# Performance work log

Hardware: AMD Instinct MI355X
Metric: run time of the kernel (lower is better)

The kernel has to match this reference:

```python
import jax, jax.numpy as jnp
import numpy as np

B = 16384
DENSE_IN = 512
N_SPARSE = 26
EMB = 128
OUT_DIM = 512
NI = N_SPARSE + 1  # 27 rows in interaction matrix
DOT_OUT = NI * (NI + 1) // 2 + DENSE_IN  # 378 + 512 = 890


def setup_inputs() -> dict:
    key = jax.random.key(0)
    ks = jax.random.split(key, 6)
    dense_tensor = jax.random.normal(ks[0], (B, DENSE_IN), dtype=jnp.float32)
    sparse_tensor = jax.random.normal(ks[1], (B, N_SPARSE, EMB), dtype=jnp.float32)
    # nn.Linear(DENSE_IN, EMB): weight [EMB, DENSE_IN], bias [EMB]
    Wp = jax.random.normal(ks[2], (EMB, DENSE_IN), dtype=jnp.float32) * (1.0 / np.sqrt(DENSE_IN))
    bp = jax.random.normal(ks[3], (EMB,), dtype=jnp.float32) * 0.01
    # nn.Linear(DOT_OUT, OUT_DIM): weight [OUT_DIM, DOT_OUT], bias [OUT_DIM]
    Wo = jax.random.normal(ks[4], (OUT_DIM, DOT_OUT), dtype=jnp.float32) * (1.0 / np.sqrt(DOT_OUT))
    bo = jax.random.normal(ks[5], (OUT_DIM,), dtype=jnp.float32) * 0.01
    return {"dense_tensor": dense_tensor, "sparse_tensor": sparse_tensor,
            "Wp": Wp, "bp": bp, "Wo": Wo, "bo": bo}


def reference(dense_tensor, sparse_tensor, Wp, bp, Wo, bo):
    # Project dense feature into embedding space (dims differ in this config)
    dense_proj = dense_tensor @ Wp.T + bp                      # [B, EMB]
    T = jnp.concatenate([dense_proj[:, None, :], sparse_tensor], axis=1)  # [B, NI, EMB]
    Z = jnp.einsum('bie,bje->bij', T, T)                       # [B, NI, NI]
    li, lj = jnp.tril_indices(NI)                              # include diagonal (offset=0)
    Zflat = Z[:, li, lj]                                       # [B, NI*(NI+1)/2]
    Zflat = jnp.concatenate([dense_tensor, Zflat], axis=-1)    # [B, DOT_OUT]
    out = Zflat @ Wo.T + bo                                    # [B, OUT_DIM]
    return out
```

## Files before the change

kernel.cpp:

```cpp
#include <hip/hip_runtime.h>

#define NB    16384
#define DIN   512
#define NSP   26
#define EMBD  128
#define NOUT  512
#define NI_   27
#define NTRI  378
#define DOTK  890
#define KPAD  896

typedef __attribute__((ext_vector_type(8)))  short bf16x8;
typedef __attribute__((ext_vector_type(4)))  float f32x4;

__device__ __forceinline__ short f2bf(float f) {
    unsigned u = __builtin_bit_cast(unsigned, f);
    unsigned r = (u + 0x7FFFu + ((u >> 16) & 1u)) >> 16;
    return (short)r;
}

__device__ __forceinline__ bf16x8 cvt8(float4 a, float4 b) {
    bf16x8 r;
    r[0] = f2bf(a.x); r[1] = f2bf(a.y); r[2] = f2bf(a.z); r[3] = f2bf(a.w);
    r[4] = f2bf(b.x); r[5] = f2bf(b.y); r[6] = f2bf(b.z); r[7] = f2bf(b.w);
    return r;
}

__device__ __forceinline__ void gld_lds16(const void* g, void* l) {
    __builtin_amdgcn_global_load_lds((const __attribute__((address_space(1))) void*)g,
                                     (__attribute__((address_space(3))) void*)l,
                                     16, 0, 0);
}

#define CONV_N2  (NB * 64)
#define WOP_N2   (NOUT * (KPAD / 8))
#define WPB_N2   (EMBD * DIN / 8)
__global__ __launch_bounds__(256) void prep_all_k(const float* __restrict__ dense,
                                                  const float* __restrict__ Wo,
                                                  const float* __restrict__ Wp,
                                                  short* __restrict__ zfb,
                                                  short* __restrict__ wop,
                                                  short* __restrict__ wpb) {
    int idx = blockIdx.x * 256 + threadIdx.x;
    if (idx < CONV_N2) {
        int b = idx >> 6, c = (idx & 63) * 8;
        const float4* p = (const float4*)(dense + (size_t)b * DIN + c);
        *(bf16x8*)(zfb + (size_t)b * KPAD + c) = cvt8(p[0], p[1]);
    } else if (idx < CONV_N2 + WOP_N2) {
        int j = idx - CONV_N2;
        int o = j / (KPAD / 8), rem = j - o * (KPAD / 8);
        int k = rem * 8;
        const float* src = Wo + (size_t)o * DOTK + k;
        bf16x8 r;
#pragma unroll
        for (int t = 0; t < 8; ++t) r[t] = (k + t < DOTK) ? f2bf(src[t]) : (short)0;
        *(bf16x8*)(wop + (size_t)o * KPAD + k) = r;
    } else {
        int j = idx - CONV_N2 - WOP_N2;
        if (j < WPB_N2) {
            const float4* p = (const float4*)(Wp + (size_t)j * 8);
            *(bf16x8*)(wpb + (size_t)j * 8) = cvt8(p[0], p[1]);
        }
    }
}

template <int BM, int BN, bool OUTBF, int GXL2>
__global__ __launch_bounds__(256) void gemm_mfma(const short* __restrict__ A, int lda,
                                                 const short* __restrict__ Bm, int ldb,
                                                 const float* __restrict__ bias,
                                                 void* __restrict__ Cp, int ldc, int K) {
    constexpr int WM = BM / 2, WN = BN / 2;
    constexpr int MT = WM / 16, NT = WN / 16;
    __shared__ short As[BM * 64];
    __shared__ short Bs[BN * 64];

    const int tid = threadIdx.x;
    const int w = tid >> 6, l = tid & 63;
    const int wm = w >> 1, wn = w & 1;
    const int r0 = l & 15, q = l >> 4;

    const int nwg = (int)(gridDim.y << GXL2);
    const int bid = ((int)blockIdx.y << GXL2) | (int)blockIdx.x;
    const int swz = (bid & 7) * (nwg >> 3) + (bid >> 3);
    const int m0 = (swz >> GXL2) * BM;
    const int n0 = (swz & ((1 << GXL2) - 1)) * BN;

    const int lr = l >> 3, pseg = l & 7;

    const f32x4 zero4 = {0.f, 0.f, 0.f, 0.f};
    f32x4 acc[MT][NT];
#pragma unroll
    for (int mi = 0; mi < MT; ++mi)
#pragma unroll
        for (int ni = 0; ni < NT; ++ni) acc[mi][ni] = zero4;

    for (int k0 = 0; k0 < K; k0 += 64) {
#pragma unroll
        for (int i = 0; i < BM / 32; ++i) {
            int r = w * (BM / 4) + i * 8 + lr;
            int ls = pseg ^ (r & 7);
            gld_lds16(A + (size_t)(m0 + r) * lda + k0 + ls * 8,
                      (char*)As + (w * (BM / 4) + i * 8) * 128);
        }
#pragma unroll
        for (int i = 0; i < BN / 32; ++i) {
            int r = w * (BN / 4) + i * 8 + lr;
            int ls = pseg ^ (r & 7);
            gld_lds16(Bm + (size_t)(n0 + r) * ldb + k0 + ls * 8,
                      (char*)Bs + (w * (BN / 4) + i * 8) * 128);
        }
        __syncthreads();

#pragma unroll
        for (int h = 0; h < 2; ++h) {
            bf16x8 af[MT], bfr[NT];
#pragma unroll
            for (int mi = 0; mi < MT; ++mi) {
                int r = wm * WM + mi * 16 + r0;
                af[mi] = *(const bf16x8*)&As[r * 64 + ((h * 4 + q) ^ (r & 7)) * 8];
            }
#pragma unroll
            for (int ni = 0; ni < NT; ++ni) {
                int r = wn * WN + ni * 16 + r0;
                bfr[ni] = *(const bf16x8*)&Bs[r * 64 + ((h * 4 + q) ^ (r & 7)) * 8];
            }
#pragma unroll
            for (int mi = 0; mi < MT; ++mi)
#pragma unroll
                for (int ni = 0; ni < NT; ++ni)
                    acc[mi][ni] = __builtin_amdgcn_mfma_f32_16x16x32_bf16(
                        af[mi], bfr[ni], acc[mi][ni], 0, 0, 0);
        }
        __syncthreads();
    }

#pragma unroll
    for (int mi = 0; mi < MT; ++mi) {
#pragma unroll
        for (int ni = 0; ni < NT; ++ni) {
            int col = n0 + wn * WN + ni * 16 + r0;
            float bb = bias[col];
#pragma unroll
            for (int r = 0; r < 4; ++r) {
                int row = m0 + wm * WM + mi * 16 + q * 4 + r;
                float v = acc[mi][ni][r] + bb;
                if (OUTBF) ((short*)Cp)[(size_t)row * ldc + col] = f2bf(v);
                else       ((float*)Cp)[(size_t)row * ldc + col] = v;
            }
        }
    }
}

__global__ __launch_bounds__(256) void interact_mfma(const float* __restrict__ sparse,
                                                     const short* __restrict__ dprojb,
                                                     short* __restrict__ zfb) {
    __shared__ short zt[4][384];
    const int w = threadIdx.x >> 6, l = threadIdx.x & 63;
    const int b = blockIdx.x * 4 + w;
    const int r0 = l & 15, q = l >> 4;

    const float* srow = sparse + (size_t)b * (NSP * EMBD);
    const short* dp = dprojb + (size_t)b * EMBD;

    const f32x4 zero4 = {0.f, 0.f, 0.f, 0.f};
    f32x4 acc00 = zero4, acc10 = zero4, acc11 = zero4;

#pragma unroll
    for (int kc = 0; kc < 4; ++kc) {
        int k = kc * 32 + q * 8;
        bf16x8 f0, f1;
        if (r0 == 0) {
            f0 = *(const bf16x8*)(dp + k);
        } else {
            const float* p = srow + (size_t)(r0 - 1) * EMBD + k;
            f0 = cvt8(*(const float4*)p, *(const float4*)(p + 4));
        }
        if (r0 <= 10) {
            const float* p = srow + (size_t)(15 + r0) * EMBD + k;
            f1 = cvt8(*(const float4*)p, *(const float4*)(p + 4));
        } else {
            f1 = (bf16x8){0, 0, 0, 0, 0, 0, 0, 0};
        }
        acc00 = __builtin_amdgcn_mfma_f32_16x16x32_bf16(f0, f0, acc00, 0, 0, 0);
        acc10 = __builtin_amdgcn_mfma_f32_16x16x32_bf16(f1, f0, acc10, 0, 0, 0);
        acc11 = __builtin_amdgcn_mfma_f32_16x16x32_bf16(f1, f1, acc11, 0, 0, 0);
    }

#pragma unroll
    for (int r = 0; r < 4; ++r) {
        int row, col;
        row = q * 4 + r;       col = r0;
        if (col <= row)             zt[w][row * (row + 1) / 2 + col] = f2bf(acc00[r]);
        row = 16 + q * 4 + r;  col = r0;
        if (row < NI_)              zt[w][row * (row + 1) / 2 + col] = f2bf(acc10[r]);
               col = 16 + r0;
        if (row < NI_ && col <= row) zt[w][row * (row + 1) / 2 + col] = f2bf(acc11[r]);
    }
    if (l < 6) zt[w][NTRI + l] = 0;
    const int* zrow = (const int*)zt[w];
    int* dst = (int*)(zfb + (size_t)b * KPAD + DIN);
#pragma unroll
    for (int t = 0; t < 3; ++t) dst[t * 64 + l] = zrow[t * 64 + l];
}

extern "C" void kernel_launch(void* const* d_in, const int* in_sizes, int n_in,
                              void* d_out, int out_size, void* d_ws, size_t ws_size,
                              hipStream_t stream) {
    const float* dense  = (const float*)d_in[0];
    const float* sparse = (const float*)d_in[1];
    const float* Wp     = (const float*)d_in[2];
    const float* bp     = (const float*)d_in[3];
    const float* Wo     = (const float*)d_in[4];
    const float* bo     = (const float*)d_in[5];
    float* out = (float*)d_out;

    short* zfb    = (short*)d_ws;
    short* dprojb = zfb + (size_t)NB * KPAD;
    short* wop    = dprojb + (size_t)NB * EMBD;
    short* wpb    = wop + (size_t)NOUT * KPAD;

    prep_all_k<<<(CONV_N2 + WOP_N2 + WPB_N2 + 255) / 256, 256, 0, stream>>>(
        dense, Wo, Wp, zfb, wop, wpb);

    gemm_mfma<64, 64, true, 1><<<dim3(EMBD / 64, NB / 64), 256, 0, stream>>>(
        zfb, KPAD, wpb, DIN, bp, dprojb, EMBD, DIN);

    interact_mfma<<<NB / 4, 256, 0, stream>>>(sparse, dprojb, zfb);

    gemm_mfma<128, 128, false, 2><<<dim3(NOUT / 128, NB / 128), 256, 0, stream>>>(
        zfb, KPAD, wop, KPAD, bo, out, NOUT, KPAD);
}
```

Measured before the change: 369.8 us.

## Fuse dense projection GEMM into interaction kernel

After: 375.3 us. About the same (+1.5%).

```diff
diff --git a/kernel.cpp b/kernel.cpp
--- a/kernel.cpp
+++ b/kernel.cpp
@@ -151,56 +151,109 @@
     }
 }
 
-__global__ __launch_bounds__(256) void interact_mfma(const float* __restrict__ sparse,
-                                                     const short* __restrict__ dprojb,
-                                                     short* __restrict__ zfb) {
-    __shared__ short zt[4][384];
+__global__ __launch_bounds__(256) void interact_fused(const float* __restrict__ sparse,
+                                                      const short* __restrict__ wpb,
+                                                      const float* __restrict__ bp,
+                                                      short* __restrict__ zfb) {
+    __shared__ union {
+        short wp[128 * 64];
+        short zt[16][384];
+    } sh;
+    __shared__ short dpl[16][128];
+
     const int w = threadIdx.x >> 6, l = threadIdx.x & 63;
-    const int b = blockIdx.x * 4 + w;
     const int r0 = l & 15, q = l >> 4;
-
-    const float* srow = sparse + (size_t)b * (NSP * EMBD);
-    const short* dp = dprojb + (size_t)b * EMBD;
+    const int b0 = blockIdx.x * 16;
+    const int lr = l >> 3, pseg = l & 7;
 
     const f32x4 zero4 = {0.f, 0.f, 0.f, 0.f};
-    f32x4 acc00 = zero4, acc10 = zero4, acc11 = zero4;
-
-#pragma unroll
-    for (int kc = 0; kc < 4; ++kc) {
-        int k = kc * 32 + q * 8;
-        bf16x8 f0, f1;
-        if (r0 == 0) {
-            f0 = *(const bf16x8*)(dp + k);
-        } else {
-            const float* p = srow + (size_t)(r0 - 1) * EMBD + k;
-            f0 = cvt8(*(const float4*)p, *(const float4*)(p + 4));
-        }
-        if (r0 <= 10) {
-            const float* p = srow + (size_t)(15 + r0) * EMBD + k;
-            f1 = cvt8(*(const float4*)p, *(const float4*)(p + 4));
-        } else {
-            f1 = (bf16x8){0, 0, 0, 0, 0, 0, 0, 0};
-        }
-        acc00 = __builtin_amdgcn_mfma_f32_16x16x32_bf16(f0, f0, acc00, 0, 0, 0);
-        acc10 = __builtin_amdgcn_mfma_f32_16x16x32_bf16(f1, f0, acc10, 0, 0, 0);
-        acc11 = __builtin_amdgcn_mfma_f32_16x16x32_bf16(f1, f1, acc11, 0, 0, 0);
-    }
-
+
+    float bb0 = bp[w * 32 + r0];
+    float bb1 = bp[w * 32 + 16 + r0];
+    f32x4 adp0 = zero4, adp1 = zero4;
+
+    for (int kc = 0; kc < 8; ++kc) {
+        int k0 = kc * 64;
+        bf16x8 af0 = *(const bf16x8*)&zfb[(size_t)(b0 + r0) * KPAD + k0 + q * 8];
+        bf16x8 af1 = *(const bf16x8*)&zfb[(size_t)(b0 + r0) * KPAD + k0 + 32 + q * 8];
+#pragma unroll
+        for (int i = 0; i < 4; ++i) {
+            int r = w * 32 + i * 8 + lr;
+            int ls = pseg ^ (r & 7);
+            gld_lds16(wpb + (size_t)r * DIN + k0 + ls * 8,
+                      (char*)sh.wp + (w * 32 + i * 8) * 128);
+        }
+        __syncthreads();
+#pragma unroll
+        for (int h = 0; h < 2; ++h) {
+            bf16x8 af = (h == 0) ? af0 : af1;
+#pragma unroll
+            for (int ni = 0; ni < 2; ++ni) {
+                int r = w * 32 + ni * 16 + r0;
+                bf16x8 bfr = *(const bf16x8*)&sh.wp[r * 64 + ((h * 4 + q) ^ (r & 7)) * 8];
+                if (ni == 0)
+                    adp0 = __builtin_amdgcn_mfma_f32_16x16x32_bf16(af, bfr, adp0, 0, 0, 0);
+                else
+                    adp1 = __builtin_amdgcn_mfma_f32_16x16x32_bf16(af, bfr, adp1, 0, 0, 0);
+            }
+        }
+        __syncthreads();
+    }
 #pragma unroll
     for (int r = 0; r < 4; ++r) {
-        int row, col;
-        row = q * 4 + r;       col = r0;
-        if (col <= row)             zt[w][row * (row + 1) / 2 + col] = f2bf(acc00[r]);
-        row = 16 + q * 4 + r;  col = r0;
-        if (row < NI_)              zt[w][row * (row + 1) / 2 + col] = f2bf(acc10[r]);
-               col = 16 + r0;
-        if (row < NI_ && col <= row) zt[w][row * (row + 1) / 2 + col] = f2bf(acc11[r]);
-    }
-    if (l < 6) zt[w][NTRI + l] = 0;
-    const int* zrow = (const int*)zt[w];
-    int* dst = (int*)(zfb + (size_t)b * KPAD + DIN);
-#pragma unroll
-    for (int t = 0; t < 3; ++t) dst[t * 64 + l] = zrow[t * 64 + l];
+        dpl[q * 4 + r][w * 32 + r0]      = f2bf(adp0[r] + bb0);
+        dpl[q * 4 + r][w * 32 + 16 + r0] = f2bf(adp1[r] + bb1);
+    }
+    __syncthreads();
+
+    for (int j = 0; j < 4; ++j) {
+        const int rloc = w * 4 + j;
+        const int b = b0 + rloc;
+        const float* srow = sparse + (size_t)b * (NSP * EMBD);
+
+        f32x4 acc00 = zero4, acc10 = zero4, acc11 = zero4;
+#pragma unroll
+        for (int kc = 0; kc < 4; ++kc) {
+            int k = kc * 32 + q * 8;
+            bf16x8 f0, f1;
+            if (r0 == 0) {
+                f0 = *(const bf16x8*)&dpl[rloc][k];
+            } else {
+                const float* p = srow + (size_t)(r0 - 1) * EMBD + k;
+                f0 = cvt8(*(const float4*)p, *(const float4*)(p + 4));
+            }
+            if (r0 <= 10) {
+                const float* p = srow + (size_t)(15 + r0) * EMBD + k;
+                f1 = cvt8(*(const float4*)p, *(const float4*)(p + 4));
+            } else {
+                f1 = (bf16x8){0, 0, 0, 0, 0, 0, 0, 0};
+            }
+            acc00 = __builtin_amdgcn_mfma_f32_16x16x32_bf16(f0, f0, acc00, 0, 0, 0);
+            acc10 = __builtin_amdgcn_mfma_f32_16x16x32_bf16(f1, f0, acc10, 0, 0, 0);
+            acc11 = __builtin_amdgcn_mfma_f32_16x16x32_bf16(f1, f1, acc11, 0, 0, 0);
+        }
+
+#pragma unroll
+        for (int r = 0; r < 4; ++r) {
+            int row, col;
+            row = q * 4 + r;       col = r0;
+            if (col <= row)              sh.zt[rloc][row * (row + 1) / 2 + col] = f2bf(acc00[r]);
+            row = 16 + q * 4 + r;  col = r0;
+            if (row < NI_)               sh.zt[rloc][row * (row + 1) / 2 + col] = f2bf(acc10[r]);
+                   col = 16 + r0;
+            if (row < NI_ && col <= row) sh.zt[rloc][row * (row + 1) / 2 + col] = f2bf(acc11[r]);
+        }
+        if (l < 6) sh.zt[rloc][NTRI + l] = 0;
+    }
+
+#pragma unroll
+    for (int j = 0; j < 4; ++j) {
+        const int rloc = w * 4 + j;
+        const int* zr = (const int*)sh.zt[rloc];
+        int* dst = (int*)(zfb + (size_t)(b0 + rloc) * KPAD + DIN);
+#pragma unroll
+        for (int t = 0; t < 3; ++t) dst[t * 64 + l] = zr[t * 64 + l];
+    }
 }
 
 extern "C" void kernel_launch(void* const* d_in, const int* in_sizes, int n_in,
@@ -214,18 +267,14 @@
     const float* bo     = (const float*)d_in[5];
     float* out = (float*)d_out;
 
-    short* zfb    = (short*)d_ws;
-    short* dprojb = zfb + (size_t)NB * KPAD;
-    short* wop    = dprojb + (size_t)NB * EMBD;
-    short* wpb    = wop + (size_t)NOUT * KPAD;
+    short* zfb = (short*)d_ws;
+    short* wop = zfb + (size_t)NB * KPAD;
+    short* wpb = wop + (size_t)NOUT * KPAD;
 
     prep_all_k<<<(CONV_N2 + WOP_N2 + WPB_N2 + 255) / 256, 256, 0, stream>>>(
         dense, Wo, Wp, zfb, wop, wpb);
 
-    gemm_mfma<64, 64, true, 1><<<dim3(EMBD / 64, NB / 64), 256, 0, stream>>>(
-        zfb, KPAD, wpb, DIN, bp, dprojb, EMBD, DIN);
-
-    interact_mfma<<<NB / 4, 256, 0, stream>>>(sparse, dprojb, zfb);
+    interact_fused<<<NB / 16, 256, 0, stream>>>(sparse, wpb, bp, zfb);
 
     gemm_mfma<128, 128, false, 2><<<dim3(NOUT / 128, NB / 128), 256, 0, stream>>>(
         zfb, KPAD, wop, KPAD, bo, out, NOUT, KPAD);
```

## Replace output GEMM with double-buffered 256x128 tile kernel using async prefetch

Applied to the files above, without the earlier changes.

New measurement: 371.1 us. About the same (+0.4%).

```diff
diff --git a/kernel.cpp b/kernel.cpp
--- a/kernel.cpp
+++ b/kernel.cpp
@@ -151,6 +151,106 @@
     }
 }
 
+__global__ __launch_bounds__(512, 2) void gemm2_deep(const short* __restrict__ A,
+                                                     const short* __restrict__ Bm,
+                                                     const float* __restrict__ bias,
+                                                     float* __restrict__ C) {
+    __shared__ short As[2][256 * 64];
+    __shared__ short Bs[2][128 * 64];
+
+    const int tid = threadIdx.x;
+    const int w = tid >> 6, l = tid & 63;
+    const int wm = w >> 1, wn = w & 1;
+    const int r0 = l & 15, q = l >> 4;
+
+    const int bid = (int)blockIdx.x;
+    const int swz = (bid & 7) * 32 + (bid >> 3);
+    const int m0 = (swz >> 2) * 256;
+    const int n0 = (swz & 3) * 128;
+
+    const int lr = l >> 3, pseg = l & 7;
+
+    auto stage = [&](int nb, int k0) {
+#pragma unroll
+        for (int i = 0; i < 4; ++i) {
+            int r = w * 32 + i * 8 + lr;
+            int ls = pseg ^ (r & 7);
+            gld_lds16(A + (size_t)(m0 + r) * KPAD + k0 + ls * 8,
+                      (char*)&As[nb][0] + (w * 32 + i * 8) * 128);
+        }
+#pragma unroll
+        for (int i = 0; i < 2; ++i) {
+            int r = w * 16 + i * 8 + lr;
+            int ls = pseg ^ (r & 7);
+            gld_lds16(Bm + (size_t)(n0 + r) * KPAD + k0 + ls * 8,
+                      (char*)&Bs[nb][0] + (w * 16 + i * 8) * 128);
+        }
+    };
+
+    const f32x4 zero4 = {0.f, 0.f, 0.f, 0.f};
+    f32x4 acc[4][4];
+#pragma unroll
+    for (int mi = 0; mi < 4; ++mi)
+#pragma unroll
+        for (int ni = 0; ni < 4; ++ni) acc[mi][ni] = zero4;
+
+    stage(0, 0);
+    stage(1, 64);
+
+    int cur = 0;
+    constexpr int NK = KPAD / 64;
+    for (int ks = 0; ks < NK; ++ks) {
+        if (ks < NK - 1) asm volatile("s_waitcnt vmcnt(6)" ::: "memory");
+        else             asm volatile("s_waitcnt vmcnt(0)" ::: "memory");
+        __builtin_amdgcn_s_barrier();
+        __builtin_amdgcn_sched_barrier(0);
+
+        __builtin_amdgcn_s_setprio(1);
+#pragma unroll
+        for (int h = 0; h < 2; ++h) {
+            bf16x8 af[4], bfr[4];
+#pragma unroll
+            for (int mi = 0; mi < 4; ++mi) {
+                int r = wm * 64 + mi * 16 + r0;
+                af[mi] = *(const bf16x8*)&As[cur][r * 64 + ((h * 4 + q) ^ (r & 7)) * 8];
+            }
+#pragma unroll
+            for (int ni = 0; ni < 4; ++ni) {
+                int r = wn * 64 + ni * 16 + r0;
+                bfr[ni] = *(const bf16x8*)&Bs[cur][r * 64 + ((h * 4 + q) ^ (r & 7)) * 8];
+            }
+#pragma unroll
+            for (int mi = 0; mi < 4; ++mi)
+#pragma unroll
+                for (int ni = 0; ni < 4; ++ni)
+                    acc[mi][ni] = __builtin_amdgcn_mfma_f32_16x16x32_bf16(
+                        af[mi], bfr[ni], acc[mi][ni], 0, 0, 0);
+        }
+        __builtin_amdgcn_s_setprio(0);
+
+        asm volatile("s_waitcnt lgkmcnt(0)" ::: "memory");
+        __builtin_amdgcn_s_barrier();
+        __builtin_amdgcn_sched_barrier(0);
+
+        if (ks + 2 < NK) stage(cur, (ks + 2) * 64);
+        cur ^= 1;
+    }
+
+#pragma unroll
+    for (int mi = 0; mi < 4; ++mi) {
+#pragma unroll
+        for (int ni = 0; ni < 4; ++ni) {
+            int col = n0 + wn * 64 + ni * 16 + r0;
+            float bb = bias[col];
+#pragma unroll
+            for (int r = 0; r < 4; ++r) {
+                int row = m0 + wm * 64 + mi * 16 + q * 4 + r;
+                C[(size_t)row * NOUT + col] = acc[mi][ni][r] + bb;
+            }
+        }
+    }
+}
+
 __global__ __launch_bounds__(256) void interact_mfma(const float* __restrict__ sparse,
                                                      const short* __restrict__ dprojb,
                                                      short* __restrict__ zfb) {
@@ -227,6 +327,5 @@
 
     interact_mfma<<<NB / 4, 256, 0, stream>>>(sparse, dprojb, zfb);
 
-    gemm_mfma<128, 128, false, 2><<<dim3(NOUT / 128, NB / 128), 256, 0, stream>>>(
-        zfb, KPAD, wop, KPAD, bo, out, NOUT, KPAD);
-}
+    gemm2_deep<<<256, 512, 0, stream>>>(zfb, wop, bo, out);
+}
```
